# Optimization experiments

Hardware: AMD Instinct MI355X
Metric: run time of the kernel (lower is better)

The kernel has to match this reference:

```python
import jax, jax.numpy as jnp
import numpy as np

N = 100000   # nodes
E = 640000   # edges
IN = 256     # raw input feature dim
D = 128      # post-MLP node feature dim (fixed in FilterGNN)


def setup_inputs() -> dict:
    key = jax.random.key(0)
    ks = jax.random.split(key, 10)
    x = jax.random.normal(ks[0], (N, IN), jnp.float32)
    alpha = jax.random.uniform(ks[1], (E, 1), jnp.float32)  # edge gate logits in [0,1)
    edge_index = jax.random.randint(ks[2], (2, E), 0, N, dtype=jnp.int32)
    norm = jnp.ones((E,), jnp.float32)  # passed to message in the original but unused
    # MLP `lin`: in_channels -> 512 -> 256 -> 128 (kaiming-normal weights, zero bias)
    def kaiming(k, fan_out, fan_in):
        return jax.random.normal(k, (fan_out, fan_in), jnp.float32) * jnp.sqrt(2.0 / fan_in)
    W1 = kaiming(ks[3], 512, IN); b1 = jnp.zeros((512,), jnp.float32)
    W2 = kaiming(ks[4], 256, 512); b2 = jnp.zeros((256,), jnp.float32)
    W3 = kaiming(ks[5], D, 256);  b3 = jnp.zeros((D,), jnp.float32)
    return {"x": x, "alpha": alpha, "edge_index": edge_index, "norm": norm,
            "W1": W1, "b1": b1, "W2": W2, "b2": b2, "W3": W3, "b3": b3}


def reference(x, alpha, edge_index, norm, W1, b1, W2, b2, W3, b3):
    # FilterGNN.lin: Linear-Tanh-Linear-Tanh-Linear  -> [N, 128]
    h = jnp.tanh(x @ W1.T + b1)
    h = jnp.tanh(h @ W2.T + b2)
    h = h @ W3.T + b3
    # FilterGraphConv1: gather x_j, elementwise relu gate, scatter-mean over targets.
    # (The [-1, H, C] view with H*C = 128 is a pure reshape; the gate broadcasts
    #  over all features, so the math is identical without the head split.)
    src, dst = edge_index[0], edge_index[1]
    gate = 2.0 * jax.nn.relu(jax.lax.stop_gradient(alpha) - 0.5)  # [E, 1]
    msg = h[src] * gate                                           # [E, 128] gather + gate
    sums = jax.ops.segment_sum(msg, dst, num_segments=N)          # [N, 128]
    cnt = jax.ops.segment_sum(jnp.ones((E,), h.dtype), dst, num_segments=N)
    out = sums / jnp.maximum(cnt, 1.0)[:, None]                   # scatter-mean (0 if no edges)
    return out
```

## Files before the change

### kernel.cpp

```cpp
#include <hip/hip_runtime.h>

typedef __attribute__((ext_vector_type(8))) short short8;
typedef __attribute__((ext_vector_type(4))) float f32x4;

__device__ __forceinline__ unsigned short f2bf(float f) {
    union { float f; unsigned u; } v; v.f = f;
    unsigned r = v.u + 0x7FFFu + ((v.u >> 16) & 1u);
    return (unsigned short)(r >> 16);
}
__device__ __forceinline__ float bf2f(unsigned short h) {
    union { unsigned u; float f; } v; v.u = ((unsigned)h) << 16;
    return v.f;
}

__device__ __forceinline__ float tanh_fast(float x) {
    float xc = fminf(fmaxf(x, -9.0f), 9.0f);
    float t  = __expf(2.0f * xc);
    return (t - 1.0f) * __builtin_amdgcn_rcpf(t + 1.0f);
}

#define GLD16(gptr, lptr)                                                     \
    __builtin_amdgcn_global_load_lds(                                         \
        (const __attribute__((address_space(1))) unsigned int*)(gptr),        \
        (__attribute__((address_space(3))) unsigned int*)(lptr), 16, 0, 0)

__global__ __launch_bounds__(256) void cast_all(
    const float* __restrict__ x,  unsigned short* __restrict__ xbf,
    const float* __restrict__ W1, unsigned short* __restrict__ w1bf,
    const float* __restrict__ W2, unsigned short* __restrict__ w2bf,
    const float* __restrict__ W3, unsigned short* __restrict__ w3bf,
    int xq)
{
    int t = blockIdx.x * 256 + threadIdx.x;
    const float* s; unsigned short* d; int q;
    if (t < xq) { s = x; d = xbf; q = t; }
    else {
        int u = t - xq;
        if (u < 32768)      { s = W1; d = w1bf; q = u; }
        else if (u < 65536) { s = W2; d = w2bf; q = u - 32768; }
        else if (u < 73728) { s = W3; d = w3bf; q = u - 65536; }
        else return;
    }
    int base = q * 4;
    float4 v = *(const float4*)(s + base);
    unsigned long long p =
        (unsigned long long)f2bf(v.x)
      | ((unsigned long long)f2bf(v.y) << 16)
      | ((unsigned long long)f2bf(v.z) << 32)
      | ((unsigned long long)f2bf(v.w) << 48);
    *(unsigned long long*)(d + base) = p;
}

#define TM 128
#define TN 128
#define BK 64

__global__ __launch_bounds__(256) void gemm_bt(
    const unsigned short* __restrict__ A, const unsigned short* __restrict__ B,
    const float* __restrict__ bias, unsigned short* __restrict__ C,
    int M, int N, int K)
{
    __shared__ __align__(16) short As[TM][BK];
    __shared__ __align__(16) short Bs[TM][BK];

    const int g  = blockIdx.x;
    const int bx = (g >> 5) * 8 + (g & 7);
    const int by = (g >> 3) & 3;
    const int mblk = (M + TM - 1) / TM;
    if (bx >= mblk) return;

    const int tid  = threadIdx.x;
    const int wave = tid >> 6;
    const int lane = tid & 63;
    const int m0 = bx * TM;
    const int n0 = by * TN;
    const int wm = (wave >> 1) * 64;
    const int wn = (wave & 1) * 64;
    const int lm = lane & 15;
    const int quad = lane >> 4;

    const int srow = lane >> 3;
    const int scol = ((lane & 7) ^ srow) * 8;
    const int cc0 = (quad ^ (lm & 7)) * 8;
    const int cc1 = ((4 + quad) ^ (lm & 7)) * 8;

    f32x4 acc[4][4] = {};

    for (int k0 = 0; k0 < K; k0 += BK) {
        #pragma unroll
        for (int i = 0; i < 4; ++i) {
            int row = wave * 32 + i * 8;
            int gr = m0 + row + srow; if (gr >= M) gr = M - 1;
            GLD16(A + (size_t)gr * K + k0 + scol, &As[row][0]);
            GLD16(B + (size_t)(n0 + row + srow) * K + k0 + scol, &Bs[row][0]);
        }
        __syncthreads();

        #pragma unroll
        for (int ks = 0; ks < BK; ks += 32) {
            const int cc = (ks == 0) ? cc0 : cc1;
            short8 af[4], bf_[4];
            #pragma unroll
            for (int i = 0; i < 4; ++i) {
                af[i]  = *(const short8*)&As[wm + i * 16 + lm][cc];
                bf_[i] = *(const short8*)&Bs[wn + i * 16 + lm][cc];
            }
            #pragma unroll
            for (int im = 0; im < 4; ++im)
                #pragma unroll
                for (int in = 0; in < 4; ++in)
                    acc[im][in] = __builtin_amdgcn_mfma_f32_16x16x32_bf16(
                        af[im], bf_[in], acc[im][in], 0, 0, 0);
        }
        __syncthreads();
    }

    #pragma unroll
    for (int im = 0; im < 4; ++im) {
        int gm_base = m0 + wm + im * 16 + quad * 4;
        #pragma unroll
        for (int in = 0; in < 4; ++in) {
            int gn = n0 + wn + in * 16 + lm;
            float bv = bias[gn];
            #pragma unroll
            for (int r = 0; r < 4; ++r) {
                int gm = gm_base + r;
                if (gm < M) {
                    float v = tanh_fast(acc[im][in][r] + bv);
                    C[(size_t)gm * N + gn] = f2bf(v);
                }
            }
        }
    }
}

__global__ __launch_bounds__(256) void gemm23_hist(
    const unsigned short* __restrict__ h1, const unsigned short* __restrict__ W2,
    const float* __restrict__ b2, const unsigned short* __restrict__ W3,
    const float* __restrict__ b3, unsigned short* __restrict__ hout, int M,
    const int* __restrict__ ei, const float* __restrict__ alpha,
    unsigned long long* __restrict__ deg, int E, int gblk)
{
    __shared__ __align__(16) short As[64][64];
    __shared__ __align__(16) short Bs[256][64];
    __shared__ __align__(16) short h2s[64][264];

    if ((int)blockIdx.x >= gblk) {
        int e = (blockIdx.x - gblk) * 256 + threadIdx.x;
        if (e < E) {
            int dst = ei[E + e];
            float gate = 2.0f * fmaxf(alpha[e] - 0.5f, 0.0f);
            atomicAdd(&deg[dst], 0x100000000ULL | (gate > 0.0f ? 1ULL : 0ULL));
        }
        return;
    }

    const int tid  = threadIdx.x;
    const int wave = tid >> 6;
    const int lane = tid & 63;
    const int m0 = blockIdx.x * 64;
    const int wm = (wave >> 1) * 32;
    const int lm = lane & 15;
    const int quad = lane >> 4;
    const int srow = lane >> 3;
    const int scol = ((lane & 7) ^ srow) * 8;
    const int cc0 = (quad ^ (lm & 7)) * 8;
    const int cc1 = ((4 + quad) ^ (lm & 7)) * 8;

    {
        const int wn = (wave & 1) * 128;
        f32x4 acc[2][8] = {};
        for (int k0 = 0; k0 < 512; k0 += 64) {
            #pragma unroll
            for (int i = 0; i < 2; ++i) {
                int r0 = wave * 16 + i * 8;
                int gr = m0 + r0 + srow; if (gr >= M) gr = M - 1;
                GLD16(h1 + (size_t)gr * 512 + k0 + scol, &As[r0][0]);
            }
            #pragma unroll
            for (int i = 0; i < 8; ++i) {
                int r0 = wave * 64 + i * 8;
                GLD16(W2 + (size_t)(r0 + srow) * 512 + k0 + scol, &Bs[r0][0]);
            }
            __syncthreads();
            #pragma unroll
            for (int ks = 0; ks < 64; ks += 32) {
                const int cc = (ks == 0) ? cc0 : cc1;
                short8 af[2], bf_[8];
                #pragma unroll
                for (int i = 0; i < 2; ++i) af[i]  = *(const short8*)&As[wm + i * 16 + lm][cc];
                #pragma unroll
                for (int i = 0; i < 8; ++i) bf_[i] = *(const short8*)&Bs[wn + i * 16 + lm][cc];
                #pragma unroll
                for (int im = 0; im < 2; ++im)
                    #pragma unroll
                    for (int in = 0; in < 8; ++in)
                        acc[im][in] = __builtin_amdgcn_mfma_f32_16x16x32_bf16(
                            af[im], bf_[in], acc[im][in], 0, 0, 0);
            }
            __syncthreads();
        }
        #pragma unroll
        for (int im = 0; im < 2; ++im) {
            int rb = wm + im * 16 + quad * 4;
            #pragma unroll
            for (int in = 0; in < 8; ++in) {
                int col = wn + in * 16 + lm;
                float bv = b2[col];
                #pragma unroll
                for (int r = 0; r < 4; ++r)
                    h2s[rb + r][col] = (short)f2bf(tanh_fast(acc[im][in][r] + bv));
            }
        }
    }
    __syncthreads();

    {
        const int wn = (wave & 1) * 64;
        short (*Bs3)[64] = (short(*)[64])&Bs[0][0];
        f32x4 acc[2][4] = {};
        for (int k0 = 0; k0 < 256; k0 += 64) {
            #pragma unroll
            for (int i = 0; i < 4; ++i) {
                int r0 = wave * 32 + i * 8;
                GLD16(W3 + (size_t)(r0 + srow) * 256 + k0 + scol, &Bs3[r0][0]);
            }
            __syncthreads();
            #pragma unroll
            for (int ks = 0; ks < 64; ks += 32) {
                const int cc = (ks == 0) ? cc0 : cc1;
                short8 af[2], bf_[4];
                #pragma unroll
                for (int i = 0; i < 2; ++i)
                    af[i] = *(const short8*)&h2s[wm + i * 16 + lm][k0 + ks + quad * 8];
                #pragma unroll
                for (int i = 0; i < 4; ++i)
                    bf_[i] = *(const short8*)&Bs3[wn + i * 16 + lm][cc];
                #pragma unroll
                for (int im = 0; im < 2; ++im)
                    #pragma unroll
                    for (int in = 0; in < 4; ++in)
                        acc[im][in] = __builtin_amdgcn_mfma_f32_16x16x32_bf16(
                            af[im], bf_[in], acc[im][in], 0, 0, 0);
            }
            __syncthreads();
        }
        #pragma unroll
        for (int im = 0; im < 2; ++im) {
            int gm_base = m0 + wm + im * 16 + quad * 4;
            #pragma unroll
            for (int in = 0; in < 4; ++in) {
                int gn = wn + in * 16 + lm;
                float bv = b3[gn];
                #pragma unroll
                for (int r = 0; r < 4; ++r) {
                    int gm = gm_base + r;
                    if (gm < M)
                        hout[(size_t)gm * 128 + gn] = f2bf(acc[im][in][r] + bv);
                }
            }
        }
    }
}

__global__ __launch_bounds__(256) void scan1(
    const unsigned long long* __restrict__ deg, int* __restrict__ rowptr,
    int* __restrict__ cursor, int* __restrict__ gcounter, int N)
{
    __shared__ int sums[256];
    __shared__ int base_sh;
    int base = blockIdx.x * 1024 + threadIdx.x * 4;
    int v[4];
    #pragma unroll
    for (int i = 0; i < 4; ++i) {
        int idx = base + i;
        v[i] = (idx < N) ? (int)(deg[idx] & 0xffffffffULL) : 0;
    }
    int s = v[0] + v[1] + v[2] + v[3];
    sums[threadIdx.x] = s;
    __syncthreads();
    for (int off = 1; off < 256; off <<= 1) {
        int t = (threadIdx.x >= off) ? sums[threadIdx.x - off] : 0;
        __syncthreads();
        sums[threadIdx.x] += t;
        __syncthreads();
    }
    int excl = sums[threadIdx.x] - s;
    if (threadIdx.x == 255) base_sh = atomicAdd(gcounter, sums[255]);
    __syncthreads();
    int run = base_sh + excl;
    #pragma unroll
    for (int i = 0; i < 4; ++i) {
        int idx = base + i;
        if (idx < N) { rowptr[idx] = run; cursor[idx] = run; }
        run += v[i];
    }
}

__global__ __launch_bounds__(256) void edge_fill(
    const int* __restrict__ ei, const float* __restrict__ alpha,
    int* __restrict__ cursor, int2* __restrict__ recs, int E)
{
    int e = blockIdx.x * 256 + threadIdx.x;
    if (e >= E) return;
    float gate = 2.0f * fmaxf(alpha[e] - 0.5f, 0.0f);
    if (gate > 0.0f) {
        int dst = ei[E + e];
        int src = ei[e];
        int pos = atomicAdd(&cursor[dst], 1);
        recs[pos] = make_int2(src, __float_as_int(gate));
    }
}

__global__ __launch_bounds__(256) void node_gather(
    const unsigned short* __restrict__ h, const unsigned long long* __restrict__ deg,
    const int* __restrict__ rowptr, const int2* __restrict__ recs,
    float* __restrict__ out, int N)
{
    int wave = threadIdx.x >> 6;
    int lane = threadIdx.x & 63;
    int node = blockIdx.x * 4 + wave;
    if (node >= N) return;
    unsigned long long d = deg[node];
    int dAll  = __builtin_amdgcn_readfirstlane((int)(d >> 32));
    int dG    = __builtin_amdgcn_readfirstlane((int)(d & 0xffffffffULL));
    int start = __builtin_amdgcn_readfirstlane(rowptr[node]);
    int qw = lane >> 4, ql = lane & 15;
    float a[8] = {};
    for (int j = 0; j < dG; j += 4) {
        int jj = j + qw;
        int idx = start + (jj < dG ? jj : dG - 1);
        int2 rec = recs[idx];
        float gate = (jj < dG) ? __int_as_float(rec.y) : 0.0f;
        uint4 u = *(const uint4*)(h + ((size_t)rec.x << 7) + ql * 8);
        a[0] += bf2f((unsigned short)(u.x & 0xffffu)) * gate;
        a[1] += bf2f((unsigned short)(u.x >> 16)) * gate;
        a[2] += bf2f((unsigned short)(u.y & 0xffffu)) * gate;
        a[3] += bf2f((unsigned short)(u.y >> 16)) * gate;
        a[4] += bf2f((unsigned short)(u.z & 0xffffu)) * gate;
        a[5] += bf2f((unsigned short)(u.z >> 16)) * gate;
        a[6] += bf2f((unsigned short)(u.w & 0xffffu)) * gate;
        a[7] += bf2f((unsigned short)(u.w >> 16)) * gate;
    }
    #pragma unroll
    for (int i = 0; i < 8; ++i) {
        a[i] += __shfl_xor(a[i], 16);
        a[i] += __shfl_xor(a[i], 32);
    }
    if (qw == 0) {
        float inv = 1.0f / fmaxf((float)dAll, 1.0f);
        float* op = out + ((size_t)node << 7) + ql * 8;
        *(float4*)(op)     = make_float4(a[0] * inv, a[1] * inv, a[2] * inv, a[3] * inv);
        *(float4*)(op + 4) = make_float4(a[4] * inv, a[5] * inv, a[6] * inv, a[7] * inv);
    }
}

extern "C" void kernel_launch(void* const* d_in, const int* in_sizes, int n_in,
                              void* d_out, int out_size, void* d_ws, size_t ws_size,
                              hipStream_t stream) {
    const float* x     = (const float*)d_in[0];
    const float* alpha = (const float*)d_in[1];
    const int*   ei    = (const int*)d_in[2];
    const float* W1 = (const float*)d_in[4];
    const float* b1 = (const float*)d_in[5];
    const float* W2 = (const float*)d_in[6];
    const float* b2 = (const float*)d_in[7];
    const float* W3 = (const float*)d_in[8];
    const float* b3 = (const float*)d_in[9];
    float* out = (float*)d_out;

    const int N = in_sizes[0] / 256;
    const int E = in_sizes[1];
    const int IN = 256, H1 = 512, D = 128;

    char* ws = (char*)d_ws;
    size_t off = 0;
    auto take = [&](size_t bytes) { char* p = ws + off; off = (off + bytes + 255) & ~(size_t)255; return p; };
    unsigned short* xbf  = (unsigned short*)take((size_t)N * IN * 2);
    unsigned short* h1bf = (unsigned short*)take((size_t)N * H1 * 2);
    unsigned short* hbf  = (unsigned short*)take((size_t)N * D  * 2);
    unsigned short* w1bf = (unsigned short*)take((size_t)H1 * IN * 2);
    unsigned short* w2bf = (unsigned short*)take((size_t)256 * H1 * 2);
    unsigned short* w3bf = (unsigned short*)take((size_t)D * 256 * 2);

    char* cbase = (char*)xbf;
    size_t coff = 0;
    auto ctake = [&](size_t bytes) { char* p = cbase + coff; coff = (coff + bytes + 255) & ~(size_t)255; return p; };
    unsigned long long* deg = (unsigned long long*)ctake((size_t)N * 8);
    int*  gcounter = (int*)ctake(256);
    int*  rowptr   = (int*)ctake((size_t)N * 4);
    int*  cursor   = (int*)ctake((size_t)N * 4);
    int2* recs     = (int2*)ctake((size_t)E * 8);

    dim3 blk(256);

    const int xq = N * IN / 4;
    const int castN = xq + 73728;
    cast_all<<<(castN + 255) / 256, blk, 0, stream>>>(x, xbf, W1, w1bf, W2, w2bf, W3, w3bf, xq);

    const int mblk = (N + TM - 1) / TM;
    const int g1 = ((mblk + 7) / 8) * 32;
    gemm_bt<<<dim3(g1), blk, 0, stream>>>(xbf, w1bf, b1, h1bf, N, H1, IN);

    hipMemsetAsync(deg, 0, (size_t)N * 8 + 256, stream);
    const int gblk = (N + 63) / 64;
    const int eblk = (E + 255) / 256;
    gemm23_hist<<<gblk + eblk, blk, 0, stream>>>(
        h1bf, w2bf, b2, w3bf, b3, hbf, N, ei, alpha, deg, E, gblk);

    const int nb1 = (N + 1023) / 1024;
    scan1<<<nb1, blk, 0, stream>>>(deg, rowptr, cursor, gcounter, N);
    edge_fill<<<eblk, blk, 0, stream>>>(ei, alpha, cursor, recs, E);

    node_gather<<<(N + 3) / 4, blk, 0, stream>>>(hbf, deg, rowptr, recs, out, N);
}
```

Measured before the change: 392.8 us.

## Fold edge histogram, scan and fill into cast and GEMM launches

Reschedules the CSR build so that each step rides along with an existing MLP kernel. The degree histogram goes into the cast kernel, the prefix scan becomes extra blocks of the first GEMM, and the edge fill becomes extra blocks of the fused second/third GEMM. This removes two standalone kernel launches and lets the graph work overlap with GEMM work. Scan state moves out of the region aliased with xbf into dedicated workspace, and the edge records now reuse the xbf buffer once layer one is done. The risk is that scan blocks inside the GEMM launch read deg written by the previous kernel, which relies on stream ordering, and that the extra blocks may delay the GEMM tails.

```diff
diff --git a/kernel.cpp b/kernel.cpp
--- a/kernel.cpp
+++ b/kernel.cpp
@@ -24,13 +24,24 @@
         (const __attribute__((address_space(1))) unsigned int*)(gptr),        \
         (__attribute__((address_space(3))) unsigned int*)(lptr), 16, 0, 0)
 
-__global__ __launch_bounds__(256) void cast_all(
+__global__ __launch_bounds__(256) void cast_hist(
     const float* __restrict__ x,  unsigned short* __restrict__ xbf,
     const float* __restrict__ W1, unsigned short* __restrict__ w1bf,
     const float* __restrict__ W2, unsigned short* __restrict__ w2bf,
     const float* __restrict__ W3, unsigned short* __restrict__ w3bf,
-    int xq)
+    int xq, int castB,
+    const int* __restrict__ ei, const float* __restrict__ alpha,
+    unsigned long long* __restrict__ deg, int E)
 {
+    if ((int)blockIdx.x >= castB) {
+        int e = (blockIdx.x - castB) * 256 + threadIdx.x;
+        if (e < E) {
+            int dst = ei[E + e];
+            float gate = 2.0f * fmaxf(alpha[e] - 0.5f, 0.0f);
+            atomicAdd(&deg[dst], 0x100000000ULL | (gate > 0.0f ? 1ULL : 0ULL));
+        }
+        return;
+    }
     int t = blockIdx.x * 256 + threadIdx.x;
     const float* s; unsigned short* d; int q;
     if (t < xq) { s = x; d = xbf; q = t; }
@@ -55,13 +66,48 @@
 #define TN 128
 #define BK 64
 
-__global__ __launch_bounds__(256) void gemm_bt(
+__global__ __launch_bounds__(256) void gemm_bt_scan(
     const unsigned short* __restrict__ A, const unsigned short* __restrict__ B,
     const float* __restrict__ bias, unsigned short* __restrict__ C,
-    int M, int N, int K)
+    int M, int N, int K,
+    const unsigned long long* __restrict__ deg, int* __restrict__ rowptr,
+    int* __restrict__ cursor, int* __restrict__ gcounter, int NN, int g1)
 {
     __shared__ __align__(16) short As[TM][BK];
     __shared__ __align__(16) short Bs[TM][BK];
+
+    if ((int)blockIdx.x >= g1) {
+        int* sums = (int*)&As[0][0];
+        int* base_sh = sums + 256;
+        int b = blockIdx.x - g1;
+        int base = b * 1024 + threadIdx.x * 4;
+        int v[4];
+        #pragma unroll
+        for (int i = 0; i < 4; ++i) {
+            int idx = base + i;
+            v[i] = (idx < NN) ? (int)(deg[idx] & 0xffffffffULL) : 0;
+        }
+        int s = v[0] + v[1] + v[2] + v[3];
+        sums[threadIdx.x] = s;
+        __syncthreads();
+        for (int off = 1; off < 256; off <<= 1) {
+            int t = (threadIdx.x >= off) ? sums[threadIdx.x - off] : 0;
+            __syncthreads();
+            sums[threadIdx.x] += t;
+            __syncthreads();
+        }
+        int excl = sums[threadIdx.x] - s;
+        if (threadIdx.x == 255) *base_sh = atomicAdd(gcounter, sums[255]);
+        __syncthreads();
+        int run = *base_sh + excl;
+        #pragma unroll
+        for (int i = 0; i < 4; ++i) {
+            int idx = base + i;
+            if (idx < NN) { rowptr[idx] = run; cursor[idx] = run; }
+            run += v[i];
+        }
+        return;
+    }
 
     const int g  = blockIdx.x;
     const int bx = (g >> 5) * 8 + (g & 7);
@@ -134,12 +180,12 @@
     }
 }
 
-__global__ __launch_bounds__(256) void gemm23_hist(
+__global__ __launch_bounds__(256) void gemm23_fill(
     const unsigned short* __restrict__ h1, const unsigned short* __restrict__ W2,
     const float* __restrict__ b2, const unsigned short* __restrict__ W3,
     const float* __restrict__ b3, unsigned short* __restrict__ hout, int M,
     const int* __restrict__ ei, const float* __restrict__ alpha,
-    unsigned long long* __restrict__ deg, int E, int gblk)
+    int* __restrict__ cursor, int2* __restrict__ recs, int E, int gblk)
 {
     __shared__ __align__(16) short As[64][64];
     __shared__ __align__(16) short Bs[256][64];
@@ -148,9 +194,13 @@
     if ((int)blockIdx.x >= gblk) {
         int e = (blockIdx.x - gblk) * 256 + threadIdx.x;
         if (e < E) {
-            int dst = ei[E + e];
             float gate = 2.0f * fmaxf(alpha[e] - 0.5f, 0.0f);
-            atomicAdd(&deg[dst], 0x100000000ULL | (gate > 0.0f ? 1ULL : 0ULL));
+            if (gate > 0.0f) {
+                int dst = ei[E + e];
+                int src = ei[e];
+                int pos = atomicAdd(&cursor[dst], 1);
+                recs[pos] = make_int2(src, __float_as_int(gate));
+            }
         }
         return;
     }
@@ -260,55 +310,6 @@
                 }
             }
         }
-    }
-}
-
-__global__ __launch_bounds__(256) void scan1(
-    const unsigned long long* __restrict__ deg, int* __restrict__ rowptr,
-    int* __restrict__ cursor, int* __restrict__ gcounter, int N)
-{
-    __shared__ int sums[256];
-    __shared__ int base_sh;
-    int base = blockIdx.x * 1024 + threadIdx.x * 4;
-    int v[4];
-    #pragma unroll
-    for (int i = 0; i < 4; ++i) {
-        int idx = base + i;
-        v[i] = (idx < N) ? (int)(deg[idx] & 0xffffffffULL) : 0;
-    }
-    int s = v[0] + v[1] + v[2] + v[3];
-    sums[threadIdx.x] = s;
-    __syncthreads();
-    for (int off = 1; off < 256; off <<= 1) {
-        int t = (threadIdx.x >= off) ? sums[threadIdx.x - off] : 0;
-        __syncthreads();
-        sums[threadIdx.x] += t;
-        __syncthreads();
-    }
-    int excl = sums[threadIdx.x] - s;
-    if (threadIdx.x == 255) base_sh = atomicAdd(gcounter, sums[255]);
-    __syncthreads();
-    int run = base_sh + excl;
-    #pragma unroll
-    for (int i = 0; i < 4; ++i) {
-        int idx = base + i;
-        if (idx < N) { rowptr[idx] = run; cursor[idx] = run; }
-        run += v[i];
-    }
-}
-
-__global__ __launch_bounds__(256) void edge_fill(
-    const int* __restrict__ ei, const float* __restrict__ alpha,
-    int* __restrict__ cursor, int2* __restrict__ recs, int E)
-{
-    int e = blockIdx.x * 256 + threadIdx.x;
-    if (e >= E) return;
-    float gate = 2.0f * fmaxf(alpha[e] - 0.5f, 0.0f);
-    if (gate > 0.0f) {
-        int dst = ei[E + e];
-        int src = ei[e];
-        int pos = atomicAdd(&cursor[dst], 1);
-        recs[pos] = make_int2(src, __float_as_int(gate));
     }
 }
 
@@ -382,35 +383,31 @@
     unsigned short* w1bf = (unsigned short*)take((size_t)H1 * IN * 2);
     unsigned short* w2bf = (unsigned short*)take((size_t)256 * H1 * 2);
     unsigned short* w3bf = (unsigned short*)take((size_t)D * 256 * 2);
-
-    char* cbase = (char*)xbf;
-    size_t coff = 0;
-    auto ctake = [&](size_t bytes) { char* p = cbase + coff; coff = (coff + bytes + 255) & ~(size_t)255; return p; };
-    unsigned long long* deg = (unsigned long long*)ctake((size_t)N * 8);
-    int*  gcounter = (int*)ctake(256);
-    int*  rowptr   = (int*)ctake((size_t)N * 4);
-    int*  cursor   = (int*)ctake((size_t)N * 4);
-    int2* recs     = (int2*)ctake((size_t)E * 8);
+    unsigned long long* deg = (unsigned long long*)take((size_t)N * 8);
+    int* gcounter = (int*)take(256);
+    int* rowptr   = (int*)take((size_t)N * 4);
+    int* cursor   = (int*)take((size_t)N * 4);
+    int2* recs = (int2*)xbf;
 
     dim3 blk(256);
 
+    hipMemsetAsync(deg, 0, (size_t)N * 8 + 256, stream);
+
     const int xq = N * IN / 4;
-    const int castN = xq + 73728;
-    cast_all<<<(castN + 255) / 256, blk, 0, stream>>>(x, xbf, W1, w1bf, W2, w2bf, W3, w3bf, xq);
+    const int castB = (xq + 73728 + 255) / 256;
+    const int eblk  = (E + 255) / 256;
+    cast_hist<<<castB + eblk, blk, 0, stream>>>(
+        x, xbf, W1, w1bf, W2, w2bf, W3, w3bf, xq, castB, ei, alpha, deg, E);
 
     const int mblk = (N + TM - 1) / TM;
     const int g1 = ((mblk + 7) / 8) * 32;
-    gemm_bt<<<dim3(g1), blk, 0, stream>>>(xbf, w1bf, b1, h1bf, N, H1, IN);
-
-    hipMemsetAsync(deg, 0, (size_t)N * 8 + 256, stream);
+    const int nb1 = (N + 1023) / 1024;
+    gemm_bt_scan<<<g1 + nb1, blk, 0, stream>>>(
+        xbf, w1bf, b1, h1bf, N, H1, IN, deg, rowptr, cursor, gcounter, N, g1);
+
     const int gblk = (N + 63) / 64;
-    const int eblk = (E + 255) / 256;
-    gemm23_hist<<<gblk + eblk, blk, 0, stream>>>(
-        h1bf, w2bf, b2, w3bf, b3, hbf, N, ei, alpha, deg, E, gblk);
-
-    const int nb1 = (N + 1023) / 1024;
-    scan1<<<nb1, blk, 0, stream>>>(deg, rowptr, cursor, gcounter, N);
-    edge_fill<<<eblk, blk, 0, stream>>>(ei, alpha, cursor, recs, E);
+    gemm23_fill<<<gblk + eblk, blk, 0, stream>>>(
+        h1bf, w2bf, b2, w3bf, b3, hbf, N, ei, alpha, cursor, recs, E, gblk);
 
     node_gather<<<(N + 3) / 4, blk, 0, stream>>>(hbf, deg, rowptr, recs, out, N);
 }
```

After: 386.3 us. Within noise of the previous version (-1.7%).
